# Kernel optimization log

Measured on AMD Instinct MI355X. Metric: run time of the kernel, lower is better.

## Reference

```python
import jax, jax.numpy as jnp
import numpy as np

N, E, IN = 50000, 800000, 128   # nodes, edges, input feature dim
H, C = 8, 32                    # heads, per-head channels
HC = H * C                      # 256 = concat width
NEG_SLOPE = 0.2
BN_EPS = 1e-5


def _gat_conv(x, src, dst, W, a_src, a_dst, b, heads, out_ch, concat):
    """PyG-style GATConv (eval mode, self-loops already in src/dst)."""
    n = x.shape[0]
    h = (x @ W).reshape(n, heads, out_ch)                 # [N,H,C]
    alpha_s = (h * a_src).sum(-1)                         # [N,H]
    alpha_d = (h * a_dst).sum(-1)                         # [N,H]
    e = jax.nn.leaky_relu(alpha_s[src] + alpha_d[dst], NEG_SLOPE)  # [Etot,H]
    # segment softmax over destination nodes (every node has a self-loop)
    emax = jax.ops.segment_max(e, dst, num_segments=n)    # [N,H]
    e = jnp.exp(e - emax[dst])
    denom = jax.ops.segment_sum(e, dst, num_segments=n)
    alpha = e / (denom[dst] + 1e-16)                      # [Etot,H]
    msg = h[src] * alpha[:, :, None]                      # [Etot,H,C]
    out = jax.ops.segment_sum(msg, dst, num_segments=n)   # [N,H,C]
    out = out.reshape(n, heads * out_ch) if concat else out.mean(axis=1)
    return out + b


def _bn(y, g, beta, m, v):
    return (y - m) * jax.lax.rsqrt(v + BN_EPS) * g + beta


def setup_inputs() -> dict:
    key = jax.random.key(0)
    ks = jax.random.split(key, 32)
    def p(i, shape, s=0.1):
        return jax.random.normal(ks[i], shape, dtype=jnp.float32) * s
    x = jax.random.normal(ks[0], (N, IN), dtype=jnp.float32)
    edge_index = jax.random.randint(ks[1], (2, E), 0, N, dtype=jnp.int32)
    d = dict(
        x=x, edge_index=edge_index,
        W1=p(2, (IN, HC)), a_src1=p(3, (H, C)), a_dst1=p(4, (H, C)), b1=p(5, (HC,)),
        bn1_g=jnp.ones((HC,), jnp.float32), bn1_b=jnp.zeros((HC,), jnp.float32),
        bn1_m=p(6, (HC,)), bn1_v=jax.random.uniform(ks[7], (HC,), jnp.float32, 0.5, 1.5),
        W2=p(8, (HC, HC)), a_src2=p(9, (H, C)), a_dst2=p(10, (H, C)), b2=p(11, (HC,)),
        bn2_g=jnp.ones((HC,), jnp.float32), bn2_b=jnp.zeros((HC,), jnp.float32),
        bn2_m=p(12, (HC,)), bn2_v=jax.random.uniform(ks[13], (HC,), jnp.float32, 0.5, 1.5),
        W3=p(14, (HC, C)), a_src3=p(15, (1, C)), a_dst3=p(16, (1, C)), b3=p(17, (C,)),
        Ws1=p(18, (IN, HC)), bs1=p(19, (HC,)),
        Ws2=p(20, (HC, C)), bs2=p(21, (C,)),
    )
    return d


def reference(x, edge_index, W1, a_src1, a_dst1, b1, bn1_g, bn1_b, bn1_m, bn1_v,
              W2, a_src2, a_dst2, b2, bn2_g, bn2_b, bn2_m, bn2_v,
              W3, a_src3, a_dst3, b3, Ws1, bs1, Ws2, bs2):
    n = x.shape[0]
    loops = jnp.arange(n, dtype=edge_index.dtype)
    src = jnp.concatenate([edge_index[0], loops])   # PyG add_self_loops=True
    dst = jnp.concatenate([edge_index[1], loops])
    x0 = x @ Ws1 + bs1                               # skip1
    h = _gat_conv(x, src, dst, W1, a_src1, a_dst1, b1, H, C, True)
    h = jax.nn.elu(_bn(h, bn1_g, bn1_b, bn1_m, bn1_v)) + x0
    xs = h @ Ws2 + bs2                               # skip2
    h2 = _gat_conv(h, src, dst, W2, a_src2, a_dst2, b2, H, C, True)
    h2 = jax.nn.elu(_bn(h2, bn2_g, bn2_b, bn2_m, bn2_v))
    out = _gat_conv(h2, src, dst, W3, a_src3, a_dst3, b3, 1, C, False) + xs
    return out
```

## Files before the change

kernel.cpp:

```cpp
#include <hip/hip_runtime.h>
#include <hip/hip_bf16.h>

#define NEG_SLOPE 0.2f
#define BN_EPS 1e-5f
#define BSH 8
#define STASH_CAP 6400

typedef __attribute__((ext_vector_type(8))) short bf16x8;
typedef __attribute__((ext_vector_type(4))) float f32x4;
typedef __attribute__((ext_vector_type(2))) float f32x2;

#if defined(__has_builtin)
#if __has_builtin(__builtin_amdgcn_cvt_f32_fp8) && __has_builtin(__builtin_amdgcn_cvt_pk_fp8_f32)
#define HW_FP8 1
#endif
#if __has_builtin(__builtin_amdgcn_cvt_pk_f32_fp8)
#define HW_FP8_PK 1
#endif
#endif

__device__ __forceinline__ float bf2f(unsigned short u) {
    union { unsigned int i; float f; } x;
    x.i = ((unsigned int)u) << 16;
    return x.f;
}
__device__ __forceinline__ unsigned short f2bf(float f) {
    __hip_bfloat16 b = __float2bfloat16(f);
    return *reinterpret_cast<unsigned short*>(&b);
}
__device__ __forceinline__ float lrelu(float v) {
    return v > 0.f ? v : NEG_SLOPE * v;
}
__device__ __forceinline__ void gload_lds16(const void* g, void* l) {
    __builtin_amdgcn_global_load_lds(
        (const __attribute__((address_space(1))) unsigned int*)(g),
        (__attribute__((address_space(3))) unsigned int*)(l),
        16, 0, 0);
}

__device__ __forceinline__ unsigned char f8enc(float f) {
#ifdef HW_FP8
    int p = __builtin_amdgcn_cvt_pk_fp8_f32(f, 0.f, 0, false);
    return (unsigned char)(p & 0xff);
#else
    float a = fabsf(f);
    unsigned int sign = (__float_as_uint(f) >> 31) << 7;
    if (a < 0.0009765625f) return (unsigned char)sign;
    a = fminf(a, 448.f);
    unsigned int bits = __float_as_uint(a);
    int e = (int)((bits >> 23) & 0xff) - 127;
    unsigned int mant = bits & 0x7fffff;
    if (e < -6) {
        int q = (int)(a * 512.f + 0.5f);
        if (q >= 8) return (unsigned char)(sign | 0x08);
        return (unsigned char)(sign | q);
    }
    unsigned int m = mant >> 20;
    unsigned int rem = mant & 0xfffff;
    if (rem > 0x80000 || (rem == 0x80000 && (m & 1))) m++;
    if (m == 8) { m = 0; e++; }
    if (e > 8) { e = 8; m = 6; }
    return (unsigned char)(sign | ((unsigned int)(e + 7) << 3) | m);
#endif
}
template <int SEL>
__device__ __forceinline__ float f8dec(unsigned int w) {
#ifdef HW_FP8
    return __builtin_amdgcn_cvt_f32_fp8(w, SEL);
#else
    unsigned int b = (w >> (SEL * 8)) & 0xff;
    unsigned int s = b >> 7, em = b & 0x7f;
    float mag;
    if (em >= 8) {
        unsigned int bits = (((em >> 3) + 120) << 23) | ((em & 7) << 20);
        mag = __uint_as_float(bits);
    } else {
        mag = (float)em * 0.001953125f;
    }
    return s ? -mag : mag;
#endif
}
__device__ __forceinline__ void fma_f8x4(float we, unsigned int wv, float4& acc) {
#ifdef HW_FP8_PK
    f32x2 lo = __builtin_amdgcn_cvt_pk_f32_fp8((int)wv, false);
    f32x2 hi = __builtin_amdgcn_cvt_pk_f32_fp8((int)wv, true);
    acc.x = fmaf(we, lo[0], acc.x);
    acc.y = fmaf(we, lo[1], acc.y);
    acc.z = fmaf(we, hi[0], acc.z);
    acc.w = fmaf(we, hi[1], acc.w);
#else
    acc.x = fmaf(we, f8dec<0>(wv), acc.x);
    acc.y = fmaf(we, f8dec<1>(wv), acc.y);
    acc.z = fmaf(we, f8dec<2>(wv), acc.z);
    acc.w = fmaf(we, f8dec<3>(wv), acc.w);
#endif
}

__device__ __forceinline__ int block_scan_incl(int v, int t) {
    int lane = t & 63, w = t >> 6;
    int sv = v;
    #pragma unroll
    for (int off = 1; off < 64; off <<= 1) {
        int u = __shfl_up(sv, off);
        if (lane >= off) sv += u;
    }
    __shared__ int ws_[4];
    if (lane == 63) ws_[w] = sv;
    __syncthreads();
    if (t == 0) {
        int a = 0;
        #pragma unroll
        for (int k = 0; k < 4; k++) { int x = ws_[k]; ws_[k] = a; a += x; }
    }
    __syncthreads();
    return sv + ws_[w];
}

__global__ __launch_bounds__(256) void phase1(const int* __restrict__ dstl,
                                              int E, int N, int NB,
                                              int* __restrict__ gHist,
                                              const float* __restrict__ x,
                                              unsigned short* __restrict__ xb, int n4x,
                                              const float* __restrict__ W1,
                                              const float* __restrict__ Ws1,
                                              const float* __restrict__ W2,
                                              const float* __restrict__ Ws2,
                                              const float* __restrict__ W3,
                                              unsigned short* __restrict__ Wcat1,
                                              unsigned short* __restrict__ Wcat2,
                                              unsigned short* __restrict__ W3t) {
    int t = threadIdx.x;
    if (blockIdx.x < 256) {
        __shared__ int h[256];
        h[t] = 0;
        __syncthreads();
        int Etot = E + N;
        for (int i = blockIdx.x * 256 + t; i < Etot; i += 256 * 256) {
            int d = (i < E) ? dstl[i] : (i - E);
            atomicAdd(&h[d >> BSH], 1);
        }
        __syncthreads();
        if (t < NB && h[t]) atomicAdd(&gHist[t], h[t]);
        return;
    }
    int i = (blockIdx.x - 256) * 256 + t;
    if (i < n4x) {
        float4 v = reinterpret_cast<const float4*>(x)[i];
        ushort4 o;
        o.x = f2bf(v.x); o.y = f2bf(v.y); o.z = f2bf(v.z); o.w = f2bf(v.w);
        reinterpret_cast<ushort4*>(xb)[i] = o;
        return;
    }
    int j = i - n4x;
    if (j < 32768) {
        int m = j >> 7, k = j & 127;
        Wcat1[j] = f2bf(W1[k * 256 + m]);
    } else if (j < 65536) {
        int q = j - 32768; int m = q >> 7, k = q & 127;
        Wcat1[32768 + q] = f2bf(Ws1[k * 256 + m]);
    } else if (j < 131072) {
        int q = j - 65536; int m = q >> 8, k = q & 255;
        Wcat2[q] = f2bf(W2[k * 256 + m]);
    } else if (j < 139264) {
        int q = j - 131072; int m = q >> 8, k = q & 255;
        Wcat2[65536 + q] = f2bf(Ws2[k * 32 + m]);
    } else if (j < 147456) {
        int q = j - 139264; int m = q >> 8, k = q & 255;
        W3t[q] = f2bf(W3[k * 32 + m]);
    }
}

__global__ __launch_bounds__(256) void bucket_scatter(const int* __restrict__ srcl,
                                                      const int* __restrict__ dstl,
                                                      int E, int N, int NB,
                                                      const int* __restrict__ gHist,
                                                      int* __restrict__ gCursor,
                                                      unsigned int* __restrict__ bktEdges) {
    __shared__ unsigned int stage[4096];
    __shared__ int lbase[256];
    __shared__ int hist[256];
    __shared__ int bexcl[257];
    __shared__ int curk[256];
    __shared__ int gbase[256];
    int t = threadIdx.x;
    int Etot = E + N;
    int begin = blockIdx.x * 4096;

    int gv = (t < NB) ? gHist[t] : 0;
    int gincl = block_scan_incl(gv, t);
    lbase[t] = gincl - gv;
    __syncthreads();

    hist[t] = 0;
    __syncthreads();

    unsigned int ent[16];
    int eb[16];
    #pragma unroll
    for (int k = 0; k < 16; k++) {
        int i = begin + k * 256 + t;
        if (i < Etot) {
            int s, d;
            if (i < E) { s = srcl[i]; d = dstl[i]; }
            else       { s = d = i - E; }
            eb[k] = d >> BSH;
            ent[k] = ((unsigned int)s << BSH) | (unsigned int)(d & 255);
            atomicAdd(&hist[eb[k]], 1);
        } else eb[k] = -1;
    }
    __syncthreads();

    int v = hist[t];
    int incl = block_scan_incl(v, t);
    bexcl[t] = incl - v;
    curk[t] = incl - v;
    if (t == 255) bexcl[256] = incl;
    __syncthreads();

    #pragma unroll
    for (int k = 0; k < 16; k++) {
        if (eb[k] >= 0) {
            int slot = atomicAdd(&curk[eb[k]], 1);
            stage[slot] = ent[k];
        }
    }
    if (t < NB) {
        int cnt = hist[t];
        gbase[t] = cnt ? (lbase[t] + atomicAdd(&gCursor[t], cnt)) : 0;
    }
    __syncthreads();

    int total = bexcl[256];
    for (int p = t; p < total; p += 256) {
        int lo = 0, hi = NB - 1;
        while (lo < hi) {
            int mid = (lo + hi + 1) >> 1;
            if (bexcl[mid] <= p) lo = mid; else hi = mid - 1;
        }
        bktEdges[gbase[lo] + (p - bexcl[lo])] = stage[p];
    }
}

__global__ __launch_bounds__(256) void bucket_to_csr(const unsigned int* __restrict__ bktEdges,
                                                     const int* __restrict__ gHist,
                                                     int* __restrict__ indptr,
                                                     int* __restrict__ esrc,
                                                     int N, int NB, int Etot) {
    __shared__ int lbase[256];
    __shared__ int nh[256];
    __shared__ int ncur[256];
    __shared__ unsigned int stash[STASH_CAP];
    int b = blockIdx.x, t = threadIdx.x;

    int gv = (t < NB) ? gHist[t] : 0;
    int gincl = block_scan_incl(gv, t);
    lbase[t] = gincl - gv;
    __syncthreads();
    int base = lbase[b];
    int cnt = gHist[b];
    int nodeBase = b << BSH;

    nh[t] = 0;
    __syncthreads();
    for (int p = t; p < cnt; p += 256) {
        unsigned int e = bktEdges[base + p];
        if (p < STASH_CAP) stash[p] = e;
        atomicAdd(&nh[e & 255], 1);
    }
    __syncthreads();
    int v = nh[t];
    int incl = block_scan_incl(v, t);
    int excl = incl - v;
    ncur[t] = excl;
    if (nodeBase + t < N) indptr[nodeBase + t] = base + excl;
    __syncthreads();
    for (int p = t; p < cnt; p += 256) {
        unsigned int e = (p < STASH_CAP) ? stash[p] : bktEdges[base + p];
        int slot = atomicAdd(&ncur[e & 255], 1);
        esrc[base + slot] = (int)(e >> BSH);
    }
    if (b == 0 && t == 0) indptr[N] = Etot;
}

__global__ __launch_bounds__(256) void gemm_tile(const unsigned short* __restrict__ A,
                                                 const unsigned short* __restrict__ Bt,
                                                 unsigned short* __restrict__ outBf,
                                                 unsigned char* __restrict__ outQ,
                                                 unsigned short* __restrict__ outSk,
                                                 const float* __restrict__ biasSk,
                                                 const float* __restrict__ aS,
                                                 const float* __restrict__ aD,
                                                 float* __restrict__ asOut,
                                                 float* __restrict__ adOut,
                                                 int M, int K, int NCtot, int split,
                                                 int ldBf, int ldSk) {
    __shared__ __align__(16) char smem[2][2][8192];
    int t = threadIdx.x;
    int w = t >> 6, lane = t & 63;
    int l16 = lane & 15, quad = lane >> 4;
    int warp_r = w >> 1, warp_c = w & 1;
    int rowBase = blockIdx.y * 128;
    int colBase = blockIdx.x * 128;

    int row_l = t & 127;
    int jchunk = t >> 7;
    int arow_st = rowBase + row_l; if (arow_st >= M) arow_st = M - 1;
    int bcol_st = colBase + row_l; if (bcol_st >= NCtot) bcol_st = NCtot - 1;
    const unsigned short* aRow = A + (size_t)arow_st * K;
    const unsigned short* bRow = Bt + (size_t)bcol_st * K;

    f32x4 acc[4][4];
    #pragma unroll
    for (int i = 0; i < 4; i++)
        #pragma unroll
        for (int j = 0; j < 4; j++) acc[i][j] = (f32x4){0.f, 0.f, 0.f, 0.f};

    auto stage = [&](int buf, int k0) {
        #pragma unroll
        for (int j = 0; j < 2; j++) {
            int chunk = j * 2 + jchunk;
            gload_lds16(aRow + k0 + chunk * 8, &smem[buf][0][(size_t)j * 4096 + (size_t)t * 16]);
            gload_lds16(bRow + k0 + chunk * 8, &smem[buf][1][(size_t)j * 4096 + (size_t)t * 16]);
        }
    };

    stage(0, 0);
    __syncthreads();
    int niter = K >> 5;
    for (int it = 0; it < niter; ++it) {
        if (it + 1 < niter) stage((it + 1) & 1, (it + 1) << 5);
        const char* Ab = &smem[it & 1][0][0];
        const char* Bb = &smem[it & 1][1][0];
        bf16x8 a[4], b[4];
        #pragma unroll
        for (int i = 0; i < 4; i++)
            a[i] = *reinterpret_cast<const bf16x8*>(Ab + quad * 2048 + (warp_r * 64 + i * 16 + l16) * 16);
        #pragma unroll
        for (int j = 0; j < 4; j++)
            b[j] = *reinterpret_cast<const bf16x8*>(Bb + quad * 2048 + (warp_c * 64 + j * 16 + l16) * 16);
        #pragma unroll
        for (int i = 0; i < 4; i++)
            #pragma unroll
            for (int j = 0; j < 4; j++)
                acc[i][j] = __builtin_amdgcn_mfma_f32_16x16x32_bf16(a[i], b[j], acc[i][j], 0, 0, 0);
        __syncthreads();
    }

    if (aS && colBase < split) {
        if (NCtot >= 128) {
            int c0 = colBase + warp_c * 64 + l16;
            int hbase = (colBase + warp_c * 64) >> 5;
            float as0 = aS[c0],      ad0 = aD[c0];
            float as1 = aS[c0 + 16], ad1 = aD[c0 + 16];
            float as2 = aS[c0 + 32], ad2 = aD[c0 + 32];
            float as3 = aS[c0 + 48], ad3 = aD[c0 + 48];
            #pragma unroll
            for (int i = 0; i < 4; i++) {
                #pragma unroll
                for (int r = 0; r < 4; r++) {
                    float va0 = acc[i][0][r] * as0 + acc[i][1][r] * as1;
                    float vd0 = acc[i][0][r] * ad0 + acc[i][1][r] * ad1;
                    float va1 = acc[i][2][r] * as2 + acc[i][3][r] * as3;
                    float vd1 = acc[i][2][r] * ad2 + acc[i][3][r] * ad3;
                    #pragma unroll
                    for (int off = 1; off < 16; off <<= 1) {
                        va0 += __shfl_xor(va0, off);
                        vd0 += __shfl_xor(vd0, off);
                        va1 += __shfl_xor(va1, off);
                        vd1 += __shfl_xor(vd1, off);
                    }
                    int row = rowBase + warp_r * 64 + i * 16 + quad * 4 + r;
                    if (l16 == 0 && row < M) {
                        asOut[row * 8 + hbase]     = va0;
                        adOut[row * 8 + hbase]     = vd0;
                        asOut[row * 8 + hbase + 1] = va1;
                        adOut[row * 8 + hbase + 1] = vd1;
                    }
                }
            }
        } else if (warp_c == 0) {
            float as0 = aS[l16],      ad0 = aD[l16];
            float as1 = aS[l16 + 16], ad1 = aD[l16 + 16];
            #pragma unroll
            for (int i = 0; i < 4; i++) {
                #pragma unroll
                for (int r = 0; r < 4; r++) {
                    float va = acc[i][0][r] * as0 + acc[i][1][r] * as1;
                    float vd = acc[i][0][r] * ad0 + acc[i][1][r] * ad1;
                    #pragma unroll
                    for (int off = 1; off < 16; off <<= 1) {
                        va += __shfl_xor(va, off);
                        vd += __shfl_xor(vd, off);
                    }
                    int row = rowBase + warp_r * 64 + i * 16 + quad * 4 + r;
                    if (l16 == 0 && row < M) {
                        asOut[row] = va;
                        adOut[row] = vd;
                    }
                }
            }
        }
    }

    #pragma unroll
    for (int i = 0; i < 4; i++) {
        #pragma unroll
        for (int r = 0; r < 4; r++) {
            int row = rowBase + warp_r * 64 + i * 16 + quad * 4 + r;
            if (row >= M) continue;
            #pragma unroll
            for (int j = 0; j < 4; j++) {
                int c = colBase + warp_c * 64 + j * 16 + l16;
                if (c >= NCtot) continue;
                float v = acc[i][j][r];
                if (c < split) {
                    if (outBf) outBf[(size_t)row * ldBf + c] = f2bf(v);
                    if (outQ)  outQ[(size_t)row * ldBf + c] = f8enc(v);
                } else {
                    outSk[(size_t)row * ldSk + (c - split)] = f2bf(v + biasSk[c - split]);
                }
            }
        }
    }
}

template <int MODE>
__global__ __launch_bounds__(256) void agg256(const unsigned char* __restrict__ hq,
                                              const float* __restrict__ as,
                                              const float* __restrict__ ad,
                                              const int* __restrict__ indptr,
                                              const int* __restrict__ esrc,
                                              const float* __restrict__ bias,
                                              const float* __restrict__ bn_g,
                                              const float* __restrict__ bn_b,
                                              const float* __restrict__ bn_m,
                                              const float* __restrict__ bn_v,
                                              const unsigned short* __restrict__ skip,
                                              unsigned short* __restrict__ out, int N) {
    int t = threadIdx.x;
    int n = blockIdx.x * 4 + (t >> 6);
    if (n >= N) return;
    int lane = t & 63;
    int e_sub = lane >> 3, h_sub = lane & 7;
    int ch_head = lane >> 3;
    int lane4 = lane * 4;
    int start = indptr[n], end = indptr[n + 1];
    int cnt = end - start;

    float adh = ad[n * 8 + h_sub];

    float4 acc = make_float4(0.f, 0.f, 0.f, 0.f);
    float sm = 0.f;
    int nfull = cnt & ~7;
    int i0 = start;
    int s_l = 0; float w8 = 0.f;
    if (nfull) {
        s_l = esrc[i0 + e_sub];
        w8 = __expf(lrelu(as[s_l * 8 + h_sub] + adh));
    }
    while (i0 < start + nfull) {
        int s_cur = s_l;
        float w_cur = w8;
        i0 += 8;
        if (i0 < start + nfull) {
            s_l = esrc[i0 + e_sub];
            w8 = __expf(lrelu(as[s_l * 8 + h_sub] + adh));
        }
        sm += w_cur;
        unsigned int hv[8];
        #pragma unroll
        for (int e = 0; e < 8; e++) {
            int se = __shfl(s_cur, e * 8);
            hv[e] = *reinterpret_cast<const unsigned int*>(&hq[(size_t)se * 256 + lane4]);
        }
        #pragma unroll
        for (int e = 0; e < 8; e++) {
            float we = __shfl(w_cur, e * 8 + ch_head);
            fma_f8x4(we, hv[e], acc);
        }
    }
    int rem = cnt - nfull;
    if (rem) {
        int idx = i0 + e_sub;
        int s_r = esrc[idx < end ? idx : end - 1];
        float w_r = (idx < end) ? __expf(lrelu(as[s_r * 8 + h_sub] + adh)) : 0.f;
        sm += w_r;
        #pragma unroll
        for (int e = 0; e < 8; e++) {
            if (e < rem) {
                int se = __shfl(s_r, e * 8);
                float we = __shfl(w_r, e * 8 + ch_head);
                unsigned int hv = *reinterpret_cast<const unsigned int*>(&hq[(size_t)se * 256 + lane4]);
                fma_f8x4(we, hv, acc);
            }
        }
    }
    #pragma unroll
    for (int off = 8; off < 64; off <<= 1) sm += __shfl_xor(sm, off);
    float il = 1.f / (sm + 1e-16f);
    float il_c = __shfl(il, ch_head);

    float4 bv  = *reinterpret_cast<const float4*>(&bias[lane4]);
    float4 gv  = *reinterpret_cast<const float4*>(&bn_g[lane4]);
    float4 bbv = *reinterpret_cast<const float4*>(&bn_b[lane4]);
    float4 mv  = *reinterpret_cast<const float4*>(&bn_m[lane4]);
    float4 vv  = *reinterpret_cast<const float4*>(&bn_v[lane4]);
    float o[4] = {acc.x * il_c + bv.x, acc.y * il_c + bv.y,
                  acc.z * il_c + bv.z, acc.w * il_c + bv.w};
    float g[4] = {gv.x, gv.y, gv.z, gv.w}, bb[4] = {bbv.x, bbv.y, bbv.z, bbv.w};
    float m[4] = {mv.x, mv.y, mv.z, mv.w}, vr[4] = {vv.x, vv.y, vv.z, vv.w};
    float sk[4] = {0.f, 0.f, 0.f, 0.f};
    if (MODE == 1) {
        ushort4 s4 = *reinterpret_cast<const ushort4*>(&skip[(size_t)n * 256 + lane4]);
        sk[0] = bf2f(s4.x); sk[1] = bf2f(s4.y); sk[2] = bf2f(s4.z); sk[3] = bf2f(s4.w);
    }
    ushort4 res;
    unsigned short* rp = &res.x;
    #pragma unroll
    for (int j = 0; j < 4; j++) {
        float val = (o[j] - m[j]) * rsqrtf(vr[j] + BN_EPS) * g[j] + bb[j];
        val = val > 0.f ? val : (__expf(val) - 1.f);
        val += sk[j];
        rp[j] = f2bf(val);
    }
    *reinterpret_cast<ushort4*>(&out[(size_t)n * 256 + lane4]) = res;
}

__global__ __launch_bounds__(256) void agg32(const unsigned short* __restrict__ h3,
                                             const float* __restrict__ as,
                                             const float* __restrict__ ad,
                                             const int* __restrict__ indptr,
                                             const int* __restrict__ esrc,
                                             const float* __restrict__ b3,
                                             const unsigned short* __restrict__ xs,
                                             float* __restrict__ out, int N) {
    int t = threadIdx.x;
    int n = blockIdx.x * 4 + (t >> 6);
    if (n >= N) return;
    int lane = t & 63;
    int e_sub = lane >> 3, c4 = (lane & 7) * 4;
    int start = indptr[n], end = indptr[n + 1];
    float adn = ad[n];

    float4 acc = make_float4(0.f, 0.f, 0.f, 0.f);
    float sm = 0.f;
    int i0 = start;
    for (; i0 + 16 <= end; i0 += 16) {
        int sA = esrc[i0 + e_sub];
        int sB = esrc[i0 + 8 + e_sub];
        float wA = __expf(lrelu(as[sA] + adn));
        float wB = __expf(lrelu(as[sB] + adn));
        sm += wA + wB;
        ushort4 hA = *reinterpret_cast<const ushort4*>(&h3[(size_t)sA * 32 + c4]);
        ushort4 hB = *reinterpret_cast<const ushort4*>(&h3[(size_t)sB * 32 + c4]);
        acc.x = fmaf(wA, bf2f(hA.x), acc.x); acc.y = fmaf(wA, bf2f(hA.y), acc.y);
        acc.z = fmaf(wA, bf2f(hA.z), acc.z); acc.w = fmaf(wA, bf2f(hA.w), acc.w);
        acc.x = fmaf(wB, bf2f(hB.x), acc.x); acc.y = fmaf(wB, bf2f(hB.y), acc.y);
        acc.z = fmaf(wB, bf2f(hB.z), acc.z); acc.w = fmaf(wB, bf2f(hB.w), acc.w);
    }
    for (; i0 < end; i0 += 8) {
        int idx = i0 + e_sub;
        bool valid = idx < end;
        if (valid) {
            int s = esrc[idx];
            float w = __expf(lrelu(as[s] + adn));
            sm += w;
            ushort4 hv = *reinterpret_cast<const ushort4*>(&h3[(size_t)s * 32 + c4]);
            acc.x = fmaf(w, bf2f(hv.x), acc.x);
            acc.y = fmaf(w, bf2f(hv.y), acc.y);
            acc.z = fmaf(w, bf2f(hv.z), acc.z);
            acc.w = fmaf(w, bf2f(hv.w), acc.w);
        }
    }
    #pragma unroll
    for (int off = 8; off < 64; off <<= 1) {
        sm    += __shfl_xor(sm, off);
        acc.x += __shfl_xor(acc.x, off);
        acc.y += __shfl_xor(acc.y, off);
        acc.z += __shfl_xor(acc.z, off);
        acc.w += __shfl_xor(acc.w, off);
    }
    if (e_sub == 0) {
        float il = 1.f / (sm + 1e-16f);
        float4 bv = *reinterpret_cast<const float4*>(&b3[c4]);
        ushort4 xv = *reinterpret_cast<const ushort4*>(&xs[(size_t)n * 32 + c4]);
        float4 o;
        o.x = acc.x * il + bv.x + bf2f(xv.x);
        o.y = acc.y * il + bv.y + bf2f(xv.y);
        o.z = acc.z * il + bv.z + bf2f(xv.z);
        o.w = acc.w * il + bv.w + bf2f(xv.w);
        *reinterpret_cast<float4*>(&out[(size_t)n * 32 + c4]) = o;
    }
}

extern "C" void kernel_launch(void* const* d_in, const int* in_sizes, int n_in,
                              void* d_out, int out_size, void* d_ws, size_t ws_size,
                              hipStream_t stream) {
    const float* x      = (const float*)d_in[0];
    const int*   eidx   = (const int*)  d_in[1];
    const float* W1     = (const float*)d_in[2];
    const float* a_src1 = (const float*)d_in[3];
    const float* a_dst1 = (const float*)d_in[4];
    const float* b1     = (const float*)d_in[5];
    const float* bn1_g  = (const float*)d_in[6];
    const float* bn1_b  = (const float*)d_in[7];
    const float* bn1_m  = (const float*)d_in[8];
    const float* bn1_v  = (const float*)d_in[9];
    const float* W2     = (const float*)d_in[10];
    const float* a_src2 = (const float*)d_in[11];
    const float* a_dst2 = (const float*)d_in[12];
    const float* b2     = (const float*)d_in[13];
    const float* bn2_g  = (const float*)d_in[14];
    const float* bn2_b  = (const float*)d_in[15];
    const float* bn2_m  = (const float*)d_in[16];
    const float* bn2_v  = (const float*)d_in[17];
    const float* W3     = (const float*)d_in[18];
    const float* a_src3 = (const float*)d_in[19];
    const float* a_dst3 = (const float*)d_in[20];
    const float* b3     = (const float*)d_in[21];
    const float* Ws1    = (const float*)d_in[22];
    const float* bs1    = (const float*)d_in[23];
    const float* Ws2    = (const float*)d_in[24];
    const float* bs2    = (const float*)d_in[25];

    const int N = in_sizes[0] / 128;
    const int E = in_sizes[1] / 2;
    const int Etot = E + N;
    const int NB = (N + 255) >> 8;
    const int* srcl = eidx;
    const int* dstl = eidx + E;

    char* ws = (char*)d_ws;
    size_t off = 0;
    auto alloc = [&](size_t bytes) -> void* {
        void* p = ws + off;
        off += (bytes + 255) & ~(size_t)255;
        return p;
    };
    unsigned short* xb    = (unsigned short*)alloc((size_t)N * 128 * 2);
    unsigned short* feat  = (unsigned short*)alloc((size_t)N * 256 * 2);
    unsigned char*  hq    = (unsigned char*)alloc((size_t)N * 256);
    unsigned short* h2b   = (unsigned short*)alloc((size_t)N * 256 * 2);
    unsigned short* featb = (unsigned short*)alloc((size_t)N * 256 * 2);
    unsigned short* xsbuf = (unsigned short*)alloc((size_t)N * 32 * 2);
    unsigned short* h3b   = (unsigned short*)alloc((size_t)N * 32 * 2);
    float*          asb   = (float*)alloc((size_t)N * 8 * 4);
    float*          adb   = (float*)alloc((size_t)N * 8 * 4);
    unsigned short* Wcat1 = (unsigned short*)alloc((size_t)512 * 128 * 2);
    unsigned short* Wcat2 = (unsigned short*)alloc((size_t)288 * 256 * 2);
    unsigned short* W3t   = (unsigned short*)alloc((size_t)32 * 256 * 2);
    int* gHC     = (int*)alloc(512 * 4);
    int* gHist   = gHC;
    int* gCursor = gHC + 256;
    unsigned int* bktEdges = (unsigned int*)alloc((size_t)Etot * 4);
    int* indptr  = (int*)alloc((size_t)(N + 1) * 4);
    int* esrc    = (int*)alloc((size_t)Etot * 4);
    (void)ws_size; (void)n_in; (void)out_size;

    hipMemsetAsync(gHC, 0, 512 * 4, stream);
    int n4x = N * 128 / 4;
    int prepBlocks = (n4x + 147456 + 255) / 256;
    phase1<<<256 + prepBlocks, 256, 0, stream>>>(dstl, E, N, NB, gHist,
                                                 x, xb, n4x,
                                                 W1, Ws1, W2, Ws2, W3,
                                                 Wcat1, Wcat2, W3t);
    bucket_scatter<<<(Etot + 4095) / 4096, 256, 0, stream>>>(srcl, dstl, E, N, NB,
                                                             gHist, gCursor, bktEdges);
    bucket_to_csr<<<NB, 256, 0, stream>>>(bktEdges, gHist, indptr, esrc, N, NB, Etot);

    int gy128 = (N + 127) / 128;
    int gn4 = (N + 3) / 4;

    gemm_tile<<<dim3(4, gy128), 256, 0, stream>>>(xb, Wcat1, nullptr, hq, feat, bs1,
                                                  a_src1, a_dst1, asb, adb,
                                                  N, 128, 512, 256, 256, 256);
    agg256<1><<<gn4, 256, 0, stream>>>(hq, asb, adb, indptr, esrc, b1,
                                       bn1_g, bn1_b, bn1_m, bn1_v, feat, h2b, N);

    gemm_tile<<<dim3(3, gy128), 256, 0, stream>>>(h2b, Wcat2, nullptr, hq, xsbuf, bs2,
                                                  a_src2, a_dst2, asb, adb,
                                                  N, 256, 288, 256, 256, 32);
    agg256<0><<<gn4, 256, 0, stream>>>(hq, asb, adb, indptr, esrc, b2,
                                       bn2_g, bn2_b, bn2_m, bn2_v, nullptr, featb, N);

    gemm_tile<<<dim3(1, gy128), 256, 0, stream>>>(featb, W3t, h3b, nullptr, h3b, nullptr,
                                                  a_src3, a_dst3, asb, adb,
                                                  N, 256, 32, 32, 32, 32);
    agg32<<<gn4, 256, 0, stream>>>(h3b, asb, adb, indptr, esrc, b3, xsbuf,
                                   (float*)d_out, N);
}
```

Baseline: 395.3 us.

## Gather fp8 rows with 16-byte loads and software-pipeline two edge batches in agg256

The 256-wide aggregation kernel now has each lane load 16 contiguous fp8 bytes (uint4) per gathered row, so four 16-lane groups each handle a different edge. Partial sums are combined afterwards with cross-group shuffle reductions. Row gathers for the next batch are issued one iteration ahead, and source indices and weights two batches ahead, to hide gather latency. This cuts the number of load instructions per edge but adds 16 accumulator registers, extra shuffle reductions, and a lane-to-channel remap for the epilogue.

```diff
diff --git a/kernel.cpp b/kernel.cpp
--- a/kernel.cpp
+++ b/kernel.cpp
@@ -441,77 +441,121 @@
     int n = blockIdx.x * 4 + (t >> 6);
     if (n >= N) return;
     int lane = t & 63;
-    int e_sub = lane >> 3, h_sub = lane & 7;
-    int ch_head = lane >> 3;
-    int lane4 = lane * 4;
+    int e8 = lane >> 3, h8 = lane & 7;
+    int g4 = lane >> 4, cl = lane & 15;
+    int hd = cl >> 1;
     int start = indptr[n], end = indptr[n + 1];
     int cnt = end - start;
 
-    float adh = ad[n * 8 + h_sub];
-
-    float4 acc = make_float4(0.f, 0.f, 0.f, 0.f);
+    float adh = ad[n * 8 + h8];
+    const unsigned char* hqc = hq + cl * 16;
+
+    float4 acc[4];
+    acc[0] = make_float4(0.f, 0.f, 0.f, 0.f);
+    acc[1] = make_float4(0.f, 0.f, 0.f, 0.f);
+    acc[2] = make_float4(0.f, 0.f, 0.f, 0.f);
+    acc[3] = make_float4(0.f, 0.f, 0.f, 0.f);
     float sm = 0.f;
     int nfull = cnt & ~7;
-    int i0 = start;
-    int s_l = 0; float w8 = 0.f;
+
+    int sA = 0, sB = 0;
+    float wA = 0.f, wB = 0.f;
+    uint4 hv0 = {}, hv1 = {};
     if (nfull) {
-        s_l = esrc[i0 + e_sub];
-        w8 = __expf(lrelu(as[s_l * 8 + h_sub] + adh));
-    }
-    while (i0 < start + nfull) {
-        int s_cur = s_l;
-        float w_cur = w8;
-        i0 += 8;
-        if (i0 < start + nfull) {
-            s_l = esrc[i0 + e_sub];
-            w8 = __expf(lrelu(as[s_l * 8 + h_sub] + adh));
-        }
-        sm += w_cur;
-        unsigned int hv[8];
-        #pragma unroll
-        for (int e = 0; e < 8; e++) {
-            int se = __shfl(s_cur, e * 8);
-            hv[e] = *reinterpret_cast<const unsigned int*>(&hq[(size_t)se * 256 + lane4]);
-        }
-        #pragma unroll
-        for (int e = 0; e < 8; e++) {
-            float we = __shfl(w_cur, e * 8 + ch_head);
-            fma_f8x4(we, hv[e], acc);
-        }
+        sA = esrc[start + e8];
+        wA = __expf(lrelu(as[sA * 8 + h8] + adh));
+        int r0 = __shfl(sA, g4 * 8);
+        int r1 = __shfl(sA, (4 + g4) * 8);
+        hv0 = *reinterpret_cast<const uint4*>(hqc + (size_t)r0 * 256);
+        hv1 = *reinterpret_cast<const uint4*>(hqc + (size_t)r1 * 256);
+        if (nfull > 8) {
+            sB = esrc[start + 8 + e8];
+            wB = __expf(lrelu(as[sB * 8 + h8] + adh));
+        }
+    }
+    for (int i0 = start; i0 < start + nfull; i0 += 8) {
+        uint4 u0 = hv0, u1 = hv1;
+        float wcur = wA;
+        if (i0 + 8 < start + nfull) {
+            int r0 = __shfl(sB, g4 * 8);
+            int r1 = __shfl(sB, (4 + g4) * 8);
+            hv0 = *reinterpret_cast<const uint4*>(hqc + (size_t)r0 * 256);
+            hv1 = *reinterpret_cast<const uint4*>(hqc + (size_t)r1 * 256);
+        }
+        sA = sB; wA = wB;
+        if (i0 + 16 < start + nfull) {
+            sB = esrc[i0 + 16 + e8];
+            wB = __expf(lrelu(as[sB * 8 + h8] + adh));
+        }
+        sm += wcur;
+        float w0 = __shfl(wcur, g4 * 8 + hd);
+        float w1 = __shfl(wcur, (4 + g4) * 8 + hd);
+        fma_f8x4(w0, u0.x, acc[0]);
+        fma_f8x4(w0, u0.y, acc[1]);
+        fma_f8x4(w0, u0.z, acc[2]);
+        fma_f8x4(w0, u0.w, acc[3]);
+        fma_f8x4(w1, u1.x, acc[0]);
+        fma_f8x4(w1, u1.y, acc[1]);
+        fma_f8x4(w1, u1.z, acc[2]);
+        fma_f8x4(w1, u1.w, acc[3]);
     }
     int rem = cnt - nfull;
     if (rem) {
-        int idx = i0 + e_sub;
-        int s_r = esrc[idx < end ? idx : end - 1];
-        float w_r = (idx < end) ? __expf(lrelu(as[s_r * 8 + h_sub] + adh)) : 0.f;
+        int i0 = start + nfull;
+        int idx = i0 + e8;
+        bool valid = idx < end;
+        int s_r = esrc[valid ? idx : end - 1];
+        float w_r = valid ? __expf(lrelu(as[s_r * 8 + h8] + adh)) : 0.f;
         sm += w_r;
-        #pragma unroll
-        for (int e = 0; e < 8; e++) {
-            if (e < rem) {
-                int se = __shfl(s_r, e * 8);
-                float we = __shfl(w_r, e * 8 + ch_head);
-                unsigned int hv = *reinterpret_cast<const unsigned int*>(&hq[(size_t)se * 256 + lane4]);
-                fma_f8x4(we, hv, acc);
-            }
-        }
+        int r0 = __shfl(s_r, g4 * 8);
+        uint4 u0 = *reinterpret_cast<const uint4*>(hqc + (size_t)r0 * 256);
+        float w0 = __shfl(w_r, g4 * 8 + hd);
+        fma_f8x4(w0, u0.x, acc[0]);
+        fma_f8x4(w0, u0.y, acc[1]);
+        fma_f8x4(w0, u0.z, acc[2]);
+        fma_f8x4(w0, u0.w, acc[3]);
+        if (rem > 4) {
+            int r1 = __shfl(s_r, (4 + g4) * 8);
+            uint4 u1 = *reinterpret_cast<const uint4*>(hqc + (size_t)r1 * 256);
+            float w1 = __shfl(w_r, (4 + g4) * 8 + hd);
+            fma_f8x4(w1, u1.x, acc[0]);
+            fma_f8x4(w1, u1.y, acc[1]);
+            fma_f8x4(w1, u1.z, acc[2]);
+            fma_f8x4(w1, u1.w, acc[3]);
+        }
+    }
+
+    #pragma unroll
+    for (int k = 0; k < 4; k++) {
+        acc[k].x += __shfl_xor(acc[k].x, 16);
+        acc[k].y += __shfl_xor(acc[k].y, 16);
+        acc[k].z += __shfl_xor(acc[k].z, 16);
+        acc[k].w += __shfl_xor(acc[k].w, 16);
+        acc[k].x += __shfl_xor(acc[k].x, 32);
+        acc[k].y += __shfl_xor(acc[k].y, 32);
+        acc[k].z += __shfl_xor(acc[k].z, 32);
+        acc[k].w += __shfl_xor(acc[k].w, 32);
     }
     #pragma unroll
     for (int off = 8; off < 64; off <<= 1) sm += __shfl_xor(sm, off);
     float il = 1.f / (sm + 1e-16f);
-    float il_c = __shfl(il, ch_head);
-
-    float4 bv  = *reinterpret_cast<const float4*>(&bias[lane4]);
-    float4 gv  = *reinterpret_cast<const float4*>(&bn_g[lane4]);
-    float4 bbv = *reinterpret_cast<const float4*>(&bn_b[lane4]);
-    float4 mv  = *reinterpret_cast<const float4*>(&bn_m[lane4]);
-    float4 vv  = *reinterpret_cast<const float4*>(&bn_v[lane4]);
-    float o[4] = {acc.x * il_c + bv.x, acc.y * il_c + bv.y,
-                  acc.z * il_c + bv.z, acc.w * il_c + bv.w};
+    float il_c = __shfl(il, hd);
+
+    float4 my = (g4 == 0) ? acc[0] : ((g4 == 1) ? acc[1] : ((g4 == 2) ? acc[2] : acc[3]));
+    int cb = cl * 16 + g4 * 4;
+
+    float4 bv  = *reinterpret_cast<const float4*>(&bias[cb]);
+    float4 gv  = *reinterpret_cast<const float4*>(&bn_g[cb]);
+    float4 bbv = *reinterpret_cast<const float4*>(&bn_b[cb]);
+    float4 mv  = *reinterpret_cast<const float4*>(&bn_m[cb]);
+    float4 vv  = *reinterpret_cast<const float4*>(&bn_v[cb]);
+    float o[4] = {my.x * il_c + bv.x, my.y * il_c + bv.y,
+                  my.z * il_c + bv.z, my.w * il_c + bv.w};
     float g[4] = {gv.x, gv.y, gv.z, gv.w}, bb[4] = {bbv.x, bbv.y, bbv.z, bbv.w};
     float m[4] = {mv.x, mv.y, mv.z, mv.w}, vr[4] = {vv.x, vv.y, vv.z, vv.w};
     float sk[4] = {0.f, 0.f, 0.f, 0.f};
     if (MODE == 1) {
-        ushort4 s4 = *reinterpret_cast<const ushort4*>(&skip[(size_t)n * 256 + lane4]);
+        ushort4 s4 = *reinterpret_cast<const ushort4*>(&skip[(size_t)n * 256 + cb]);
         sk[0] = bf2f(s4.x); sk[1] = bf2f(s4.y); sk[2] = bf2f(s4.z); sk[3] = bf2f(s4.w);
     }
     ushort4 res;
@@ -523,7 +567,7 @@
         val += sk[j];
         rp[j] = f2bf(val);
     }
-    *reinterpret_cast<ushort4*>(&out[(size_t)n * 256 + lane4]) = res;
+    *reinterpret_cast<ushort4*>(&out[(size_t)n * 256 + cb]) = res;
 }
 
 __global__ __launch_bounds__(256) void agg32(const unsigned short* __restrict__ h3,
```

Measured after the change: 542.4 us. 37.2% more time.
